# Kernel tuning notes

Hardware: AMD Instinct MI355X
Metric: run time of the kernel (lower is better)

## Reference

```python
import jax, jax.numpy as jnp
import numpy as np

B, K, DIN, D, NH, HD, FF = 16384, 64, 49, 16, 2, 8, 32
EPS = 1e-5


def _ln(x, g, b):
    m = jnp.mean(x, axis=-1, keepdims=True)
    v = jnp.mean((x - m) ** 2, axis=-1, keepdims=True)
    return (x - m) / jnp.sqrt(v + EPS) * g + b


def setup_inputs() -> dict:
    key = jax.random.key(0)
    ks = jax.random.split(key, 20)
    s = 0.05
    return {
        "x": jax.random.normal(ks[0], (B, K, DIN), dtype=jnp.float32),
        # torch Linear layout: weight is [out, in]
        "proj_w": jax.random.normal(ks[1], (D, DIN), dtype=jnp.float32) * s,
        "proj_b": jax.random.normal(ks[2], (D,), dtype=jnp.float32) * s,
        "pos": jax.random.normal(ks[3], (1, K, D), dtype=jnp.float32) * s,
        "in_proj_w": jax.random.normal(ks[4], (3 * D, D), dtype=jnp.float32) * s,
        "in_proj_b": jax.random.normal(ks[5], (3 * D,), dtype=jnp.float32) * s,
        "out_w": jax.random.normal(ks[6], (D, D), dtype=jnp.float32) * s,
        "out_b": jax.random.normal(ks[7], (D,), dtype=jnp.float32) * s,
        "ln1_g": jnp.ones((D,), dtype=jnp.float32),
        "ln1_b": jnp.zeros((D,), dtype=jnp.float32),
        "lin1_w": jax.random.normal(ks[8], (FF, D), dtype=jnp.float32) * s,
        "lin1_b": jax.random.normal(ks[9], (FF,), dtype=jnp.float32) * s,
        "lin2_w": jax.random.normal(ks[10], (D, FF), dtype=jnp.float32) * s,
        "lin2_b": jax.random.normal(ks[11], (D,), dtype=jnp.float32) * s,
        "ln2_g": jnp.ones((D,), dtype=jnp.float32),
        "ln2_b": jnp.zeros((D,), dtype=jnp.float32),
        "head_w": jax.random.normal(ks[12], (1, D), dtype=jnp.float32) * s,
        "head_b": jax.random.normal(ks[13], (1,), dtype=jnp.float32) * s,
    }


def reference(x, proj_w, proj_b, pos, in_proj_w, in_proj_b, out_w, out_b,
              ln1_g, ln1_b, lin1_w, lin1_b, lin2_w, lin2_b, ln2_g, ln2_b,
              head_w, head_b):
    # input projection + learned positional embedding
    h = jnp.einsum("bki,di->bkd", x, proj_w) + proj_b + pos  # [B,K,D]

    # --- self-attention (torch MultiheadAttention, post-norm encoder layer) ---
    qkv = jnp.einsum("bkd,ed->bke", h, in_proj_w) + in_proj_b  # [B,K,3D]
    q, k, v = jnp.split(qkv, 3, axis=-1)
    q = q.reshape(B, K, NH, HD)
    k = k.reshape(B, K, NH, HD)
    v = v.reshape(B, K, NH, HD)
    scores = jnp.einsum("bqhd,bkhd->bhqk", q, k) / jnp.sqrt(jnp.float32(HD))
    attn = jax.nn.softmax(scores, axis=-1)
    ctx = jnp.einsum("bhqk,bkhd->bqhd", attn, v).reshape(B, K, D)
    attn_out = jnp.einsum("bkd,od->bko", ctx, out_w) + out_b
    h = _ln(h + attn_out, ln1_g, ln1_b)

    # --- FFN (relu), post-norm ---
    ff = jnp.einsum("bkd,fd->bkf", h, lin1_w) + lin1_b
    ff = jax.nn.relu(ff)
    ff = jnp.einsum("bkf,df->bkd", ff, lin2_w) + lin2_b
    h = _ln(h + ff, ln2_g, ln2_b)

    # mean pool over sequence, then scalar head
    pooled = h.mean(axis=1)  # [B,D]
    out = jnp.einsum("bd,od->bo", pooled, head_w) + head_b
    return out.squeeze(-1)  # [B]
```

## Files before the change

### kernel.cpp

```cpp
#include <hip/hip_runtime.h>


#define SCALE 0.510069729f

#define KRS   24
#define VTB   1536
#define VTS   72
#define HRB   6304
#define HRS   40
#define RED   8864
#define SMTOT 8872

#define WS_HB   2304
#define WS_EP   3328

typedef __bf16 v8bf __attribute__((ext_vector_type(8)));
typedef float  v4f  __attribute__((ext_vector_type(4)));

#define LDS_ORDER() __asm__ volatile("" ::: "memory")

static __device__ __forceinline__ short f2bs(float f) {
    __bf16 h = (__bf16)f;
    return __builtin_bit_cast(short, h);
}
#define MFMA(a,b,c) __builtin_amdgcn_mfma_f32_16x16x32_bf16((a),(b),(c),0,0,0)

template<int IMM> static __device__ __forceinline__ float swz(float x) {
    return __builtin_bit_cast(float,
        __builtin_amdgcn_ds_swizzle(__builtin_bit_cast(int, x), IMM));
}

static __device__ __forceinline__ void red16(v4f& v) {
    #pragma unroll
    for (int r = 0; r < 4; ++r) v[r] += swz<0x041F>(v[r]);
    #pragma unroll
    for (int r = 0; r < 4; ++r) v[r] += swz<0x081F>(v[r]);
    #pragma unroll
    for (int r = 0; r < 4; ++r) v[r] += swz<0x101F>(v[r]);
    #pragma unroll
    for (int r = 0; r < 4; ++r) v[r] += swz<0x201F>(v[r]);
}

__global__ __launch_bounds__(64)
void tx_prep(const float* __restrict__ proj_w, const float* __restrict__ proj_b,
             const float* __restrict__ pos,
             const float* __restrict__ in_proj_w, const float* __restrict__ in_proj_b,
             const float* __restrict__ out_w, const float* __restrict__ out_b,
             const float* __restrict__ ln1_g, const float* __restrict__ ln1_b,
             const float* __restrict__ lin1_w, const float* __restrict__ lin1_b,
             const float* __restrict__ lin2_w, const float* __restrict__ lin2_b,
             const float* __restrict__ ln2_g, const float* __restrict__ ln2_b,
             const float* __restrict__ head_w, float* __restrict__ ws)
{
    const int lane = threadIdx.x, g = lane >> 4, c = lane & 15;
    v8bf* wf = (v8bf*)ws;
    v8bf F;
    #pragma unroll
    for (int j = 0; j < 8; ++j) F[j] = (__bf16)proj_w[c*49 + g*8 + j];
    wf[0*64 + lane] = F;
    #pragma unroll
    for (int j = 0; j < 8; ++j) { int k = 32 + g*8 + j; F[j] = (k < 49) ? (__bf16)proj_w[c*49 + k] : (__bf16)0.f; }
    wf[1*64 + lane] = F;
    #pragma unroll
    for (int nt = 0; nt < 3; ++nt) {
        #pragma unroll
        for (int j = 0; j < 8; ++j) { int k = g*8 + j; F[j] = (k < 16) ? (__bf16)in_proj_w[(nt*16 + c)*16 + k] : (__bf16)0.f; }
        wf[(2 + nt)*64 + lane] = F;
    }
    #pragma unroll
    for (int j = 0; j < 8; ++j) { int k = g*8 + j; F[j] = (k < 16) ? (__bf16)out_w[c*16 + k] : (__bf16)0.f; }
    wf[5*64 + lane] = F;
    #pragma unroll
    for (int nt = 0; nt < 2; ++nt) {
        #pragma unroll
        for (int j = 0; j < 8; ++j) { int k = g*8 + j; F[j] = (k < 16) ? (__bf16)lin1_w[(nt*16 + c)*16 + k] : (__bf16)0.f; }
        wf[(6 + nt)*64 + lane] = F;
    }
    #pragma unroll
    for (int j = 0; j < 8; ++j) F[j] = (__bf16)lin2_w[c*32 + g*8 + j];
    wf[8*64 + lane] = F;

    float* hb = ws + WS_HB;
    #pragma unroll
    for (int ww = 0; ww < 4; ++ww)
        #pragma unroll
        for (int r = 0; r < 4; ++r)
            hb[ww*256 + lane*4 + r] = proj_b[c] + pos[(ww*16 + g*4 + r)*16 + c];

    if (lane < 16) {
        float* ep = ws + WS_EP + lane*16;
        ep[0]  = in_proj_b[lane];
        ep[1]  = in_proj_b[16 + lane] * SCALE;
        ep[2]  = in_proj_b[32 + lane];
        ep[3]  = out_b[lane];
        ep[4]  = ln1_g[lane];
        ep[5]  = ln1_b[lane];
        ep[6]  = lin1_b[lane];
        ep[7]  = lin1_b[16 + lane];
        ep[8]  = lin2_b[lane];
        ep[9]  = ln2_g[lane];
        ep[10] = ln2_b[lane];
        ep[11] = head_w[lane];
        ep[12] = 0.f; ep[13] = 0.f; ep[14] = 0.f; ep[15] = 0.f;
    }
}

__global__ __launch_bounds__(256, 8)
void tx_main(const float* __restrict__ x, const float* __restrict__ ws,
             const float* __restrict__ head_b, float* __restrict__ out)
{
    __shared__ __align__(16) short sm[SMTOT];
    const int tid   = threadIdx.x;
    const int w     = tid >> 6;
    const int lane  = tid & 63;
    const int g     = lane >> 4;
    const int c     = lane & 15;
    const int b     = blockIdx.x;
    const int myrow = w*16 + c;
    const int tok0  = w*16 + g*4;
    const v8bf* wf  = (const v8bf*)ws;
    const float4* ep4 = (const float4*)(ws + WS_EP);
    float* smf = (float*)sm;

    v8bf zfrag;
    #pragma unroll
    for (int j = 0; j < 8; ++j) zfrag[j] = (__bf16)0.f;
    const v4f zacc = {0.f, 0.f, 0.f, 0.f};

    const float4* xb4 = (const float4*)(x + (size_t)b * 3136);
    float4* sf4 = (float4*)smf;
    #pragma unroll
    for (int i = 0; i < 3; ++i) sf4[tid + i*256] = xb4[tid + i*256];
    if (tid < 16)      sf4[768 + tid] = xb4[768 + tid];
    else if (tid < 32) smf[3136 + tid - 16] = 0.f;
    *(unsigned long long*)&sm[HRB + myrow*HRS + 16 + g*4] = 0ull;
    __syncthreads();

    v4f hC;
    {
        const float* xr = smf + myrow*49 + g*8;
        v8bf a0, a1;
        #pragma unroll
        for (int j = 0; j < 8; ++j) a0[j] = (__bf16)xr[j];
        #pragma unroll
        for (int j = 0; j < 8; ++j) a1[j] = (__bf16)xr[32 + j];
        v4f hb = ((const v4f*)(ws + WS_HB))[w*64 + lane];
        hC = MFMA(a0, wf[0*64 + lane], hb);
        hC = MFMA(a1, wf[1*64 + lane], hC);
        #pragma unroll
        for (int r = 0; r < 4; ++r) sm[HRB + (tok0 + r)*HRS + c] = f2bs(hC[r]);
    }
    __syncthreads();

    {
        if (tid < 64) {
            float4 z4 = {0.f, 0.f, 0.f, 0.f};
            *(float4*)&sm[tid*KRS + 16] = z4;
        }
        v8bf a = *(const v8bf*)&sm[HRB + myrow*HRS + g*8];
        v4f qC = MFMA(a, wf[2*64 + lane], zacc);
        v4f kC = MFMA(a, wf[3*64 + lane], zacc);
        v4f vC = MFMA(a, wf[4*64 + lane], zacc);
        float4 e0 = ep4[c*4];
        const int vsl = VTB + c*VTS + 32*(w >> 1) + 8*g + 4*(w & 1);
        #pragma unroll
        for (int r = 0; r < 4; ++r) {
            int tok = tok0 + r;
            sm[HRB + tok*HRS + c] = f2bs(qC[r] + e0.x);
            sm[tok*KRS + c]       = f2bs(fmaf(kC[r], SCALE, e0.y));
            sm[vsl + r]           = f2bs(vC[r] + e0.z);
        }
    }
    __syncthreads();

    v4f ctxC0, ctxC1;
    {
        v8bf aq = *(const v8bf*)&sm[HRB + myrow*HRS + g*8];
        #pragma unroll
        for (int hh = 0; hh < 2; ++hh) {
            v8bf bq = (g == hh) ? aq : zfrag;
            v8bf plo, phi;
            {
                v8bf ak0 = *(const v8bf*)&sm[(0*16 + c)*KRS + g*8];
                v8bf ak1 = *(const v8bf*)&sm[(1*16 + c)*KRS + g*8];
                v4f s0 = MFMA(ak0, bq, zacc);
                v4f s1 = MFMA(ak1, bq, zacc);
                #pragma unroll
                for (int r = 0; r < 4; ++r) {
                    plo[r]     = (__bf16)__builtin_amdgcn_exp2f(s0[r]);
                    plo[4 + r] = (__bf16)__builtin_amdgcn_exp2f(s1[r]);
                }
                v8bf ak2 = *(const v8bf*)&sm[(2*16 + c)*KRS + g*8];
                v8bf ak3 = *(const v8bf*)&sm[(3*16 + c)*KRS + g*8];
                v4f s2 = MFMA(ak2, bq, zacc);
                v4f s3 = MFMA(ak3, bq, zacc);
                #pragma unroll
                for (int r = 0; r < 4; ++r) {
                    phi[r]     = (__bf16)__builtin_amdgcn_exp2f(s2[r]);
                    phi[4 + r] = (__bf16)__builtin_amdgcn_exp2f(s3[r]);
                }
            }
            v8bf bv0 = zfrag, bv1 = zfrag;
            bool act  = (hh == 0) ? (c < 8) : (c >= 8);
            int  onec = (hh == 0) ? 8 : 7;
            if (act) {
                bv0 = *(const v8bf*)&sm[VTB + c*VTS + g*8];
                bv1 = *(const v8bf*)&sm[VTB + c*VTS + 32 + g*8];
            } else if (c == onec) {
                #pragma unroll
                for (int j = 0; j < 8; ++j) { bv0[j] = (__bf16)1.f; bv1[j] = (__bf16)1.f; }
            }
            v4f acc = MFMA(plo, bv0, zacc);
            acc = MFMA(phi, bv1, acc);
            if (hh) ctxC1 = acc; else ctxC0 = acc;
        }
    }

    {
        #pragma unroll
        for (int r = 0; r < 4; ++r) {
            float l0 = swz<0x110>(ctxC0[r]);
            float l1 = swz<0x0F0>(ctxC1[r]);
            float num = (c < 8) ? ctxC0[r] : ctxC1[r];
            float den = (c < 8) ? l0 : l1;
            sm[HRB + (tok0 + r)*HRS + c] = f2bs(num * __builtin_amdgcn_rcpf(den));
        }
    }
    LDS_ORDER();

    v4f hln;
    {
        v8bf a = *(const v8bf*)&sm[HRB + myrow*HRS + g*8];
        v4f oC = MFMA(a, wf[5*64 + lane], hC);
        float4 e0 = ep4[c*4];
        float4 e1 = ep4[c*4 + 1];
        v4f hn, s, q;
        #pragma unroll
        for (int r = 0; r < 4; ++r) { hn[r] = oC[r] + e0.w; s[r] = hn[r]; q[r] = hn[r]*hn[r]; }
        red16(s);
        red16(q);
        #pragma unroll
        for (int r = 0; r < 4; ++r) {
            float mean = s[r]*0.0625f;
            float var  = fmaf(q[r], 0.0625f, -mean*mean);
            float is = __builtin_amdgcn_rsqf(var + 1e-5f);
            hln[r] = (hn[r] - mean)*is*e1.x + e1.y;
            sm[HRB + (tok0 + r)*HRS + c] = f2bs(hln[r]);
        }
    }
    LDS_ORDER();

    v4f o2;
    {
        v8bf a = *(const v8bf*)&sm[HRB + myrow*HRS + g*8];
        v4f f0 = MFMA(a, wf[6*64 + lane], zacc);
        v4f f1 = MFMA(a, wf[7*64 + lane], zacc);
        float4 e1 = ep4[c*4 + 1];
        #pragma unroll
        for (int r = 0; r < 4; ++r) {
            int tok = tok0 + r;
            sm[HRB + tok*HRS + c]      = f2bs(fmaxf(f0[r] + e1.z, 0.f));
            sm[HRB + tok*HRS + 16 + c] = f2bs(fmaxf(f1[r] + e1.w, 0.f));
        }
        LDS_ORDER();
        v8bf a2 = *(const v8bf*)&sm[HRB + myrow*HRS + g*8];
        o2 = MFMA(a2, wf[8*64 + lane], hln);
    }

    float part = 0.f;
    {
        float4 e2 = ep4[c*4 + 2];
        v4f hn, s, q;
        #pragma unroll
        for (int r = 0; r < 4; ++r) { hn[r] = o2[r] + e2.x; s[r] = hn[r]; q[r] = hn[r]*hn[r]; }
        red16(s);
        red16(q);
        #pragma unroll
        for (int r = 0; r < 4; ++r) {
            float mean = s[r]*0.0625f;
            float var  = fmaf(q[r], 0.0625f, -mean*mean);
            float is = __builtin_amdgcn_rsqf(var + 1e-5f);
            float h3 = (hn[r] - mean)*is*e2.y + e2.z;
            part = fmaf(h3, e2.w, part);
        }
    }
    part += swz<0x041F>(part);
    part += swz<0x081F>(part);
    part += swz<0x101F>(part);
    part += swz<0x201F>(part);
    part += swz<0x401F>(part);
    part += __shfl_xor(part, 32, 64);
    float* fred = (float*)&sm[RED];
    if (lane == 0) fred[w] = part;
    __syncthreads();
    if (tid == 0)
        out[b] = (fred[0] + fred[1] + fred[2] + fred[3]) * (1.f/64.f) + head_b[0];
}

extern "C" void kernel_launch(void* const* d_in, const int* in_sizes, int n_in,
                              void* d_out, int out_size, void* d_ws, size_t ws_size,
                              hipStream_t stream) {
    const float* x         = (const float*)d_in[0];
    const float* proj_w    = (const float*)d_in[1];
    const float* proj_b    = (const float*)d_in[2];
    const float* pos       = (const float*)d_in[3];
    const float* in_proj_w = (const float*)d_in[4];
    const float* in_proj_b = (const float*)d_in[5];
    const float* out_w     = (const float*)d_in[6];
    const float* out_b     = (const float*)d_in[7];
    const float* ln1_g     = (const float*)d_in[8];
    const float* ln1_b     = (const float*)d_in[9];
    const float* lin1_w    = (const float*)d_in[10];
    const float* lin1_b    = (const float*)d_in[11];
    const float* lin2_w    = (const float*)d_in[12];
    const float* lin2_b    = (const float*)d_in[13];
    const float* ln2_g     = (const float*)d_in[14];
    const float* ln2_b     = (const float*)d_in[15];
    const float* head_w    = (const float*)d_in[16];
    const float* head_b    = (const float*)d_in[17];
    float* ws = (float*)d_ws;

    tx_prep<<<1, 64, 0, stream>>>(proj_w, proj_b, pos, in_proj_w, in_proj_b,
                                  out_w, out_b, ln1_g, ln1_b, lin1_w, lin1_b,
                                  lin2_w, lin2_b, ln2_g, ln2_b, head_w, ws);
    tx_main<<<16384, 256, 0, stream>>>(x, ws, head_b, (float*)d_out);
}
```

Baseline: 327.9 us.

## Load input rows directly from global memory instead of staging through LDS

Each lane now reads its input row fragments straight from global memory rather than cooperatively copying the whole 64x49 tile into shared memory first. This removes two block-wide barriers and roughly halves the LDS footprint, so more blocks can be resident per CU. The second K-slice is clamped to an offset of 41 and the repacked proj_w fragment is rearranged so the overlapping columns get zero weight. The per-lane global reads are unaligned, strided scalar loads that coalesce worse than the old float4 copy. The layernorm variance is also folded into one fused fma chain.

```diff
diff --git a/kernel.cpp b/kernel.cpp
--- a/kernel.cpp
+++ b/kernel.cpp
@@ -6,10 +6,10 @@
 #define KRS   24
 #define VTB   1536
 #define VTS   72
-#define HRB   6304
+#define HRB   2688
 #define HRS   40
-#define RED   8864
-#define SMTOT 8872
+#define RED   5248
+#define SMTOT 5256
 
 #define WS_HB   2304
 #define WS_EP   3328
@@ -59,7 +59,11 @@
     for (int j = 0; j < 8; ++j) F[j] = (__bf16)proj_w[c*49 + g*8 + j];
     wf[0*64 + lane] = F;
     #pragma unroll
-    for (int j = 0; j < 8; ++j) { int k = 32 + g*8 + j; F[j] = (k < 49) ? (__bf16)proj_w[c*49 + k] : (__bf16)0.f; }
+    for (int j = 0; j < 8; ++j) {
+        int k = (g == 0) ? (32 + j) : (g == 1) ? (40 + j)
+              : (g == 2 && j == 7) ? 48 : -1;
+        F[j] = (k >= 0) ? (__bf16)proj_w[c*49 + k] : (__bf16)0.f;
+    }
     wf[1*64 + lane] = F;
     #pragma unroll
     for (int nt = 0; nt < 3; ++nt) {
@@ -120,43 +124,36 @@
     const int tok0  = w*16 + g*4;
     const v8bf* wf  = (const v8bf*)ws;
     const float4* ep4 = (const float4*)(ws + WS_EP);
-    float* smf = (float*)sm;
 
     v8bf zfrag;
     #pragma unroll
     for (int j = 0; j < 8; ++j) zfrag[j] = (__bf16)0.f;
     const v4f zacc = {0.f, 0.f, 0.f, 0.f};
 
-    const float4* xb4 = (const float4*)(x + (size_t)b * 3136);
-    float4* sf4 = (float4*)smf;
-    #pragma unroll
-    for (int i = 0; i < 3; ++i) sf4[tid + i*256] = xb4[tid + i*256];
-    if (tid < 16)      sf4[768 + tid] = xb4[768 + tid];
-    else if (tid < 32) smf[3136 + tid - 16] = 0.f;
     *(unsigned long long*)&sm[HRB + myrow*HRS + 16 + g*4] = 0ull;
-    __syncthreads();
+    if (lane < 16) {
+        float4 z4 = {0.f, 0.f, 0.f, 0.f};
+        *(float4*)&sm[(w*16 + lane)*KRS + 16] = z4;
+    }
 
     v4f hC;
     {
-        const float* xr = smf + myrow*49 + g*8;
+        const float* xr = x + (size_t)b * 3136 + myrow*49;
+        int off1 = 32 + g*8; if (off1 > 41) off1 = 41;
         v8bf a0, a1;
         #pragma unroll
-        for (int j = 0; j < 8; ++j) a0[j] = (__bf16)xr[j];
-        #pragma unroll
-        for (int j = 0; j < 8; ++j) a1[j] = (__bf16)xr[32 + j];
+        for (int j = 0; j < 8; ++j) a0[j] = (__bf16)xr[g*8 + j];
+        #pragma unroll
+        for (int j = 0; j < 8; ++j) a1[j] = (__bf16)xr[off1 + j];
         v4f hb = ((const v4f*)(ws + WS_HB))[w*64 + lane];
         hC = MFMA(a0, wf[0*64 + lane], hb);
         hC = MFMA(a1, wf[1*64 + lane], hC);
         #pragma unroll
         for (int r = 0; r < 4; ++r) sm[HRB + (tok0 + r)*HRS + c] = f2bs(hC[r]);
     }
-    __syncthreads();
-
-    {
-        if (tid < 64) {
-            float4 z4 = {0.f, 0.f, 0.f, 0.f};
-            *(float4*)&sm[tid*KRS + 16] = z4;
-        }
+    LDS_ORDER();
+
+    {
         v8bf a = *(const v8bf*)&sm[HRB + myrow*HRS + g*8];
         v4f qC = MFMA(a, wf[2*64 + lane], zacc);
         v4f kC = MFMA(a, wf[3*64 + lane], zacc);
@@ -242,8 +239,7 @@
         #pragma unroll
         for (int r = 0; r < 4; ++r) {
             float mean = s[r]*0.0625f;
-            float var  = fmaf(q[r], 0.0625f, -mean*mean);
-            float is = __builtin_amdgcn_rsqf(var + 1e-5f);
+            float is = __builtin_amdgcn_rsqf(fmaf(q[r], 0.0625f, fmaf(mean, -mean, 1e-5f)));
             hln[r] = (hn[r] - mean)*is*e1.x + e1.y;
             sm[HRB + (tok0 + r)*HRS + c] = f2bs(hln[r]);
         }
@@ -278,8 +274,7 @@
         #pragma unroll
         for (int r = 0; r < 4; ++r) {
             float mean = s[r]*0.0625f;
-            float var  = fmaf(q[r], 0.0625f, -mean*mean);
-            float is = __builtin_amdgcn_rsqf(var + 1e-5f);
+            float is = __builtin_amdgcn_rsqf(fmaf(q[r], 0.0625f, fmaf(mean, -mean, 1e-5f)));
             float h3 = (hn[r] - mean)*is*e2.y + e2.z;
             part = fmaf(h3, e2.w, part);
         }
```

After: 324.2 us. Within noise of the previous version (-1.1%).
